# Kernel tuning notes

Hardware: AMD Instinct MI355X
Metric: run time of the kernel (lower is better)

Reference implementation:

```python
import jax, jax.numpy as jnp
import numpy as np

B, CTX, QST, E, H = 8, 4096, 512, 300, 128

def setup_inputs() -> dict:
    key = jax.random.key(0)
    k1, k2, k3, k4 = jax.random.split(key, 4)
    context_sequence = jax.random.normal(k1, (B, CTX, E), dtype=jnp.float32)
    question_sequence = jax.random.normal(k2, (B, QST, E), dtype=jnp.float32)
    question_mask = jnp.ones((B, QST), dtype=jnp.int32)
    # dense layer params (PyTorch Linear: y = x @ W.T + b)
    bound = 1.0 / np.sqrt(E)
    W = jax.random.uniform(k3, (H, E), minval=-bound, maxval=bound, dtype=jnp.float32)
    b = jax.random.uniform(k4, (H,), minval=-bound, maxval=bound, dtype=jnp.float32)
    return {"context_sequence": context_sequence, "question_sequence": question_sequence,
            "question_mask": question_mask, "W": W, "b": b}

def reference(context_sequence, question_sequence, question_mask, W, b):
    # ReLU(dense(x)) for both sequences
    ctx_logits = jax.nn.relu(jnp.einsum('bce,he->bch', context_sequence, W) + b)   # [B, CTX, H]
    qst_logits = jax.nn.relu(jnp.einsum('bqe,he->bqh', question_sequence, W) + b)  # [B, QST, H]
    scores = jnp.einsum('bch,bqh->bcq', ctx_logits, qst_logits)                    # [B, CTX, QST]
    scores = jnp.where(question_mask[:, None, :] == 0, -jnp.inf, scores)
    attn = jax.nn.softmax(scores, axis=-1)
    return jnp.einsum('bcq,bqh->bch', attn, qst_logits)                            # [B, CTX, H]
```

## Files before the change

kernel.cpp:

```cpp
#include <hip/hip_runtime.h>
#include <hip/hip_bf16.h>

#define BB   8
#define SCTX 4096
#define SQ   512
#define EE   300
#define HH   128
#define CST  328
#define LOG2E 1.4426950408889634f

typedef short bhalf4 __attribute__((ext_vector_type(4)));
typedef short short8 __attribute__((ext_vector_type(8)));
typedef float f32x4  __attribute__((ext_vector_type(4)));
typedef unsigned u32x4 __attribute__((ext_vector_type(4)));

#define MFMA16(a, b, c) __builtin_amdgcn_mfma_f32_16x16x32_bf16((a), (b), (c), 0, 0, 0)
#define SBAR()   __builtin_amdgcn_s_barrier()
#define SCHED0() __builtin_amdgcn_sched_barrier(0)

__device__ __forceinline__ short f2bf(float f) {
  unsigned u = __builtin_bit_cast(unsigned, f);
  u += 0x7fffu + ((u >> 16) & 1u);
  return (short)(u >> 16);
}
__device__ __forceinline__ float bf2f(short s) {
  return __builtin_bit_cast(float, ((unsigned)(unsigned short)s) << 16);
}
__device__ __forceinline__ unsigned pack2(float a, float b) {
  return (unsigned)(unsigned short)f2bf(a) | ((unsigned)(unsigned short)f2bf(b) << 16);
}
__device__ __forceinline__ void gload16(const void* g, void* lds) {
  __builtin_amdgcn_global_load_lds(
      (const __attribute__((address_space(1))) void*)g,
      (__attribute__((address_space(3))) void*)lds, 16, 0, 0);
}

__global__ __launch_bounds__(256) void k_qlog(const float* __restrict__ qst,
                                              const float* __restrict__ W,
                                              const float* __restrict__ bias,
                                              short* __restrict__ ql,
                                              short* __restrict__ qlT,
                                              short* __restrict__ wsw) {
  const int b = blockIdx.y;
  const int q0 = blockIdx.x * 16;
  const int tid = threadIdx.x;
  const int w = tid >> 6, l = tid & 63, t = l & 15, quad = l >> 4;

  __shared__ __align__(16) short cst[16 * CST];

  const float4* cbase = (const float4*)(qst + (size_t)(b * SQ + q0) * EE);
#pragma unroll
  for (int j = 0; j < 5; ++j) {
    int i4 = tid + j * 256;
    if (i4 < 1200) {
      float4 v = cbase[i4];
      int row = i4 / 75, c4 = i4 - row * 75;
      bhalf4 s4; s4[0] = f2bf(v.x); s4[1] = f2bf(v.y); s4[2] = f2bf(v.z); s4[3] = f2bf(v.w);
      *(bhalf4*)(cst + row * CST + c4 * 4) = s4;
    }
  }
  for (int i = tid; i < 160; i += 256) {
    int row = i / 10, c = (i - row * 10) * 2;
    *(int*)&cst[row * CST + 300 + c] = 0;
  }
  if (b == 0) {
    const int h = blockIdx.x * 4;
#pragma unroll
    for (int j = 0; j < 5; ++j) {
      int i = tid + j * 256;
      int hi = i / 320, k = i - hi * 320;
      float v = (k < EE) ? W[(h + hi) * EE + k] : 0.0f;
      int m = (h + hi) >> 4, tt = (h + hi) & 15, kk = k >> 5, qq = (k >> 3) & 3, jj = k & 7;
      wsw[((kk * 8 + m) * 64 + qq * 16 + tt) * 8 + jj] = f2bf(v);
    }
  }
  __syncthreads();

  f32x4 acc1[2] = {}, acc2[2] = {};
  const short* arow = cst + t * CST;
#pragma unroll
  for (int kk = 0; kk < 10; ++kk) {
    short8 a = *(const short8*)(arow + kk * 32 + quad * 8);
#pragma unroll
    for (int n = 0; n < 2; ++n) {
      const int habs = (w * 2 + n) * 16;
      short8 w8;
      if (kk < 9) {
        const float* wrow = W + (size_t)(habs + t) * EE + kk * 32 + quad * 8;
        float4 f0 = *(const float4*)(wrow);
        float4 f1 = *(const float4*)(wrow + 4);
        w8[0] = f2bf(f0.x); w8[1] = f2bf(f0.y); w8[2] = f2bf(f0.z); w8[3] = f2bf(f0.w);
        w8[4] = f2bf(f1.x); w8[5] = f2bf(f1.y); w8[6] = f2bf(f1.z); w8[7] = f2bf(f1.w);
      } else {
#pragma unroll
        for (int jj = 0; jj < 8; ++jj) {
          int k = 288 + quad * 8 + jj;
          w8[jj] = (k < EE) ? f2bf(W[(size_t)(habs + t) * EE + k]) : (short)0;
        }
      }
      acc1[n] = MFMA16(a, w8, acc1[n]);
      acc2[n] = MFMA16(w8, a, acc2[n]);
    }
  }
#pragma unroll
  for (int n = 0; n < 2; ++n) {
    const int habs = (w * 2 + n) * 16;
    const float bv1 = bias[habs + t];
    bhalf4 s1;
#pragma unroll
    for (int r = 0; r < 4; ++r) s1[r] = f2bf(fmaxf(acc1[n][r] + bv1, 0.0f));
    *(bhalf4*)&qlT[((size_t)b * HH + habs + t) * SQ + q0 + quad * 4] = s1;
    const float4 bv2 = *(const float4*)(bias + habs + quad * 4);
    bhalf4 s2;
    s2[0] = f2bf(fmaxf(acc2[n][0] + bv2.x, 0.0f));
    s2[1] = f2bf(fmaxf(acc2[n][1] + bv2.y, 0.0f));
    s2[2] = f2bf(fmaxf(acc2[n][2] + bv2.z, 0.0f));
    s2[3] = f2bf(fmaxf(acc2[n][3] + bv2.w, 0.0f));
    *(bhalf4*)&ql[((size_t)b * SQ + q0 + t) * HH + habs + quad * 4] = s2;
  }
}

__global__ __launch_bounds__(256, 2) void k_attn(const float* __restrict__ ctx,
                                                 const short* __restrict__ wsw,
                                                 const float* __restrict__ bias,
                                                 const int* __restrict__ mask,
                                                 const short* __restrict__ ql,
                                                 const short* __restrict__ qlT,
                                                 float* __restrict__ out) {
  const int b = blockIdx.y;
  const int m0 = blockIdx.x * 64;
  const int tid = threadIdx.x;
  const int w = tid >> 6, l = tid & 63, t = l & 15, quad = l >> 4;
  const int g = w >> 1, hf = w & 1;

  __shared__ __align__(16) short uq[16384];
  __shared__ __align__(16) short uv[16384];
  __shared__ __align__(16) short maskh[SQ];
  short* cst = uq;
  short* clt = uv;
  short* qb0 = uq;          short* qb1 = uq + 8192;
  short* vb0 = uv;          short* vb1 = uv + 8192;

  for (int i = tid; i < SQ; i += 256)
    maskh[i] = f2bf(mask[b * SQ + i] ? -8.0f : -1e30f);

  for (int i = 0; i < 2; ++i) {
    const float4* cbase = (const float4*)(ctx + ((size_t)b * SCTX + m0 + i * 32) * EE);
#pragma unroll
    for (int j = 0; j < 10; ++j) {
      int i4 = tid + j * 256;
      if (i4 < 2400) {
        float4 v = cbase[i4];
        int row = i4 / 75, c4 = i4 - row * 75;
        bhalf4 s4; s4[0] = f2bf(v.x); s4[1] = f2bf(v.y); s4[2] = f2bf(v.z); s4[3] = f2bf(v.w);
        *(bhalf4*)(cst + row * CST + c4 * 4) = s4;
      }
    }
    for (int k = tid; k < 320; k += 256) {
      int row = k / 10, c = (k - row * 10) * 2;
      *(int*)&cst[row * CST + 300 + c] = 0;
    }
    __syncthreads();
    const short* arow = cst + (g * 16 + t) * CST;
    f32x4 acc[4] = {};
#pragma unroll
    for (int kk = 0; kk < 10; ++kk) {
      const int k = kk * 32 + quad * 8;
      short8 a = *(const short8*)(arow + k);
      short8 w8[4];
#pragma unroll
      for (int n = 0; n < 4; ++n)
        w8[n] = *(const short8*)(wsw + ((kk * 8 + hf * 4 + n) * 64 + l) * 8);
#pragma unroll
      for (int n = 0; n < 4; ++n) acc[n] = MFMA16(a, w8[n], acc[n]);
    }
#pragma unroll
    for (int n = 0; n < 4; ++n) {
      const int h = (hf * 4 + n) * 16 + t;
      const float bv = bias[h];
#pragma unroll
      for (int r = 0; r < 4; ++r) {
        float v = fmaxf(acc[n][r] + bv, 0.0f);
        clt[(i * 32 + g * 16 + quad * 4 + r) * 136 + h] = f2bf(v);
      }
    }
    __syncthreads();
  }

  short8 af[4];
#pragma unroll
  for (int kk = 0; kk < 4; ++kk)
    af[kk] = *(const short8*)&clt[(w * 16 + t) * 136 + kk * 32 + quad * 8];
  __syncthreads();

  const int srcA = ((quad & 1) * 2) * 16 + t;
  const int srcB = srcA + 16;
  const bool hiq = quad >= 2;
  const int sx  = (t & 7) << 3;
  const int rl4 = l >> 4;
  const int cbq = (l & 15) * 16;
  const int rl8 = l >> 3;
  const int cbv = (l & 7) * 16;

  auto stageTo = [&](short* qb, short* vb, int c) {
#pragma unroll
    for (int s = 0; s < 4; ++s) {
      const int row = w * 16 + s * 4 + rl4;
      gload16((const char*)(ql + ((size_t)b * SQ + c * 64 + row) * HH) +
                  (cbq ^ ((row & 7) << 4)),
              qb + (w * 16 + s * 4) * 128);
    }
#pragma unroll
    for (int s = 0; s < 4; ++s) {
      const int row = w * 32 + s * 8 + rl8;
      gload16((const char*)(qlT + ((size_t)b * HH + row) * SQ + c * 64) +
                  (cbv ^ ((row & 7) << 4)),
              vb + (w * 32 + s * 8) * 64);
    }
  };

  stageTo(qb0, vb0, 0);
  stageTo(qb1, vb1, 1);

  f32x4 o[8] = {};
  float rtot = 0.0f;
  for (int c = 0; c < 8; ++c) {
    short* qch = (c & 1) ? qb1 : qb0;
    short* vch = (c & 1) ? vb1 : vb0;
    if (c < 7) { asm volatile("s_waitcnt vmcnt(8)" ::: "memory"); }
    else       { asm volatile("s_waitcnt vmcnt(0)" ::: "memory"); }
    SCHED0(); SBAR(); SCHED0();

    f32x4 sv[4] = {};
#pragma unroll
    for (int n2 = 0; n2 < 4; ++n2) {
      const short* qr = qch + (n2 * 16 + t) * 128;
#pragma unroll
      for (int kx = 0; kx < 4; ++kx) {
        short8 b8 = *(const short8*)(qr + ((kx * 32 + quad * 8) ^ sx));
        sv[n2] = MFMA16(b8, af[kx], sv[n2]);
      }
    }
    unsigned pk[8];
#pragma unroll
    for (int n2 = 0; n2 < 4; ++n2) {
      bhalf4 mb = *(const bhalf4*)&maskh[c * 64 + n2 * 16 + quad * 4];
      float p0 = exp2f((sv[n2][0] + bf2f(mb[0])) * LOG2E);
      float p1 = exp2f((sv[n2][1] + bf2f(mb[1])) * LOG2E);
      float p2 = exp2f((sv[n2][2] + bf2f(mb[2])) * LOG2E);
      float p3 = exp2f((sv[n2][3] + bf2f(mb[3])) * LOG2E);
      rtot += (p0 + p1) + (p2 + p3);
      pk[n2 * 2 + 0] = pack2(p0, p1);
      pk[n2 * 2 + 1] = pack2(p2, p3);
    }
    unsigned sA[8], sB[8];
#pragma unroll
    for (int i = 0; i < 8; ++i) {
      sA[i] = (unsigned)__shfl((int)pk[i], srcA);
      sB[i] = (unsigned)__shfl((int)pk[i], srcB);
    }
#pragma unroll
    for (int kk2 = 0; kk2 < 2; ++kk2) {
      u32x4 av;
      av[0] = hiq ? sA[kk2 * 4 + 2] : sA[kk2 * 4 + 0];
      av[1] = hiq ? sA[kk2 * 4 + 3] : sA[kk2 * 4 + 1];
      av[2] = hiq ? sB[kk2 * 4 + 2] : sB[kk2 * 4 + 0];
      av[3] = hiq ? sB[kk2 * 4 + 3] : sB[kk2 * 4 + 1];
      short8 pa = __builtin_bit_cast(short8, av);
      const int co = (kk2 * 32 + quad * 8) ^ sx;
#pragma unroll
      for (int n = 0; n < 8; ++n) {
        short8 v8 = *(const short8*)&vch[(n * 16 + t) * 64 + co];
        o[n] = MFMA16(pa, v8, o[n]);
      }
    }
    if (c < 7) {
      asm volatile("s_waitcnt lgkmcnt(0)" ::: "memory");
      SCHED0(); SBAR(); SCHED0();
      if (c < 6) stageTo(qch, vch, c + 2);
    }
  }

  rtot += __shfl_xor(rtot, 16);
  rtot += __shfl_xor(rtot, 32);
  f32x4 rinv;
#pragma unroll
  for (int r = 0; r < 4; ++r) rinv[r] = 1.0f / __shfl(rtot, quad * 4 + r);
  float* obase = out + ((size_t)b * SCTX + m0 + w * 16) * HH;
#pragma unroll
  for (int n = 0; n < 8; ++n)
#pragma unroll
    for (int r = 0; r < 4; ++r)
      obase[(quad * 4 + r) * HH + n * 16 + t] = o[n][r] * rinv[r];
}

extern "C" void kernel_launch(void* const* d_in, const int* in_sizes, int n_in,
                              void* d_out, int out_size, void* d_ws, size_t ws_size,
                              hipStream_t stream) {
  const float* ctx  = (const float*)d_in[0];
  const float* qst  = (const float*)d_in[1];
  const int*   mask = (const int*)d_in[2];
  const float* W    = (const float*)d_in[3];
  const float* bias = (const float*)d_in[4];
  float* out = (float*)d_out;

  short* wsw  = (short*)d_ws;
  short* ql   = (short*)((char*)d_ws + 81920);
  short* qlT  = ql + (size_t)BB * SQ * HH;

  k_qlog<<<dim3(SQ / 16, BB), dim3(256), 0, stream>>>(qst, W, bias, ql, qlT, wsw);
  k_attn<<<dim3(SCTX / 64, BB), dim3(256), 0, stream>>>(ctx, wsw, bias, mask, ql, qlT, out);
}
```

Before: 124.5 us.

## Prepack W in separate kernel and simplify attention staging to single-barrier prefetch

Moves the bf16 swizzled packing of W into its own small kernel, so k_qlog reads prepacked bf16 fragments instead of converting fp32 W per block. In the attention kernel, the two-deep prefetch with hand-placed vmcnt waits and two barriers per chunk becomes one __syncthreads per chunk followed by a prefetch of only the next chunk. This trades a shallower load-compute overlap and an extra kernel launch for less per-block conversion work and simpler synchronisation.

```diff
diff --git a/kernel.cpp b/kernel.cpp
--- a/kernel.cpp
+++ b/kernel.cpp
@@ -6,6 +6,7 @@
 #define SQ   512
 #define EE   300
 #define HH   128
+#define EP   320
 #define CST  328
 #define LOG2E 1.4426950408889634f
 
@@ -15,8 +16,6 @@
 typedef unsigned u32x4 __attribute__((ext_vector_type(4)));
 
 #define MFMA16(a, b, c) __builtin_amdgcn_mfma_f32_16x16x32_bf16((a), (b), (c), 0, 0, 0)
-#define SBAR()   __builtin_amdgcn_s_barrier()
-#define SCHED0() __builtin_amdgcn_sched_barrier(0)
 
 __device__ __forceinline__ short f2bf(float f) {
   unsigned u = __builtin_bit_cast(unsigned, f);
@@ -35,12 +34,18 @@
       (__attribute__((address_space(3))) void*)lds, 16, 0, 0);
 }
 
+__global__ void k_wpad(const float* __restrict__ W, short* __restrict__ wsw) {
+  const int h = blockIdx.x, k = threadIdx.x;
+  float v = (k < EE) ? W[h * EE + k] : 0.0f;
+  const int m = h >> 4, t = h & 15, kk = k >> 5, quad = (k >> 3) & 3, j = k & 7;
+  wsw[((kk * 8 + m) * 64 + quad * 16 + t) * 8 + j] = f2bf(v);
+}
+
 __global__ __launch_bounds__(256) void k_qlog(const float* __restrict__ qst,
-                                              const float* __restrict__ W,
+                                              const short* __restrict__ wsw,
                                               const float* __restrict__ bias,
                                               short* __restrict__ ql,
-                                              short* __restrict__ qlT,
-                                              short* __restrict__ wsw) {
+                                              short* __restrict__ qlT) {
   const int b = blockIdx.y;
   const int q0 = blockIdx.x * 16;
   const int tid = threadIdx.x;
@@ -63,17 +68,6 @@
     int row = i / 10, c = (i - row * 10) * 2;
     *(int*)&cst[row * CST + 300 + c] = 0;
   }
-  if (b == 0) {
-    const int h = blockIdx.x * 4;
-#pragma unroll
-    for (int j = 0; j < 5; ++j) {
-      int i = tid + j * 256;
-      int hi = i / 320, k = i - hi * 320;
-      float v = (k < EE) ? W[(h + hi) * EE + k] : 0.0f;
-      int m = (h + hi) >> 4, tt = (h + hi) & 15, kk = k >> 5, qq = (k >> 3) & 3, jj = k & 7;
-      wsw[((kk * 8 + m) * 64 + qq * 16 + tt) * 8 + jj] = f2bf(v);
-    }
-  }
   __syncthreads();
 
   f32x4 acc1[2] = {}, acc2[2] = {};
@@ -83,21 +77,8 @@
     short8 a = *(const short8*)(arow + kk * 32 + quad * 8);
 #pragma unroll
     for (int n = 0; n < 2; ++n) {
-      const int habs = (w * 2 + n) * 16;
-      short8 w8;
-      if (kk < 9) {
-        const float* wrow = W + (size_t)(habs + t) * EE + kk * 32 + quad * 8;
-        float4 f0 = *(const float4*)(wrow);
-        float4 f1 = *(const float4*)(wrow + 4);
-        w8[0] = f2bf(f0.x); w8[1] = f2bf(f0.y); w8[2] = f2bf(f0.z); w8[3] = f2bf(f0.w);
-        w8[4] = f2bf(f1.x); w8[5] = f2bf(f1.y); w8[6] = f2bf(f1.z); w8[7] = f2bf(f1.w);
-      } else {
-#pragma unroll
-        for (int jj = 0; jj < 8; ++jj) {
-          int k = 288 + quad * 8 + jj;
-          w8[jj] = (k < EE) ? f2bf(W[(size_t)(habs + t) * EE + k]) : (short)0;
-        }
-      }
+      const int m = w * 2 + n;
+      short8 w8 = *(const short8*)(wsw + ((kk * 8 + m) * 64 + l) * 8);
       acc1[n] = MFMA16(a, w8, acc1[n]);
       acc2[n] = MFMA16(w8, a, acc2[n]);
     }
@@ -220,16 +201,14 @@
   };
 
   stageTo(qb0, vb0, 0);
-  stageTo(qb1, vb1, 1);
 
   f32x4 o[8] = {};
   float rtot = 0.0f;
   for (int c = 0; c < 8; ++c) {
     short* qch = (c & 1) ? qb1 : qb0;
     short* vch = (c & 1) ? vb1 : vb0;
-    if (c < 7) { asm volatile("s_waitcnt vmcnt(8)" ::: "memory"); }
-    else       { asm volatile("s_waitcnt vmcnt(0)" ::: "memory"); }
-    SCHED0(); SBAR(); SCHED0();
+    __syncthreads();
+    if (c < 7) stageTo((c & 1) ? qb0 : qb1, (c & 1) ? vb0 : vb1, c + 1);
 
     f32x4 sv[4] = {};
 #pragma unroll
@@ -274,11 +253,6 @@
         o[n] = MFMA16(pa, v8, o[n]);
       }
     }
-    if (c < 7) {
-      asm volatile("s_waitcnt lgkmcnt(0)" ::: "memory");
-      SCHED0(); SBAR(); SCHED0();
-      if (c < 6) stageTo(qch, vch, c + 2);
-    }
   }
 
   rtot += __shfl_xor(rtot, 16);
@@ -308,6 +282,7 @@
   short* ql   = (short*)((char*)d_ws + 81920);
   short* qlT  = ql + (size_t)BB * SQ * HH;
 
-  k_qlog<<<dim3(SQ / 16, BB), dim3(256), 0, stream>>>(qst, W, bias, ql, qlT, wsw);
+  k_wpad<<<dim3(HH), dim3(EP), 0, stream>>>(W, wsw);
+  k_qlog<<<dim3(SQ / 16, BB), dim3(256), 0, stream>>>(qst, wsw, bias, ql, qlT);
   k_attn<<<dim3(SCTX / 64, BB), dim3(256), 0, stream>>>(ctx, wsw, bias, mask, ql, qlT, out);
 }
```

Result: faster. 117.6 us (-5.6%).
